# Optimization experiments

Hardware: AMD Instinct MI355X
Metric: run time of the kernel (lower is better)

The kernel has to match this reference:

```python
import jax, jax.numpy as jnp
import numpy as np
import math

INF = 1e10

def setup_inputs() -> dict:
    key = jax.random.key(0)
    ks = jax.random.split(key, 6)
    B, S, T, D = 8, 1024, 1024, 1024
    stdv = 1.0 / math.sqrt(D)
    return {
        "key": jax.random.normal(ks[0], (B, S, D), dtype=jnp.float32),
        "mask_src": jnp.ones((B, S), dtype=jnp.float32),
        "mask_trg": jnp.ones((B, T), dtype=jnp.float32),
        "Wq": jax.random.uniform(ks[1], (D, D), jnp.float32, -stdv, stdv),
        "bq": jnp.zeros((D,), jnp.float32),
        "Wk": jax.random.uniform(ks[2], (D, D), jnp.float32, -stdv, stdv),
        "bk": jnp.zeros((D,), jnp.float32),
        "wg": jax.random.uniform(ks[3], (D,), jnp.float32, -stdv, stdv),
        "bg": jnp.zeros((1,), jnp.float32),
    }


def reference(key, mask_src, mask_trg, Wq, bq, Wk, bk, wg, bg):
    B, S, D = key.shape
    T = mask_trg.shape[1]
    scale = jnp.asarray(math.sqrt(D), key.dtype)

    # --- linear (position-based Gaussian) attention ---
    src_lens = mask_src.sum(-1)                      # [B]
    trg_lens = mask_trg.sum(-1)                      # [B]
    steps = src_lens / trg_lens                      # [B]
    idx_t = steps[:, None] * jnp.arange(T, dtype=key.dtype)[None, :]   # [B,T]
    idx_s = jnp.arange(S, dtype=key.dtype)                              # [S]
    dist2 = (idx_s[None, None, :] - idx_t[:, :, None]) ** 2            # [B,T,S]
    l_logits = -dist2 / 0.3 - INF * (1.0 - mask_src[:, None, :])
    l_att = jax.nn.softmax(l_logits, axis=-1)                           # [B,T,S]

    # query from position attention
    query = jnp.einsum('bts,bsd->btd', l_att, key)                      # [B,T,D]

    # learned gate, broadcast [B,T,1] -> [B,T,S]
    gates = jax.nn.sigmoid(query @ wg + bg)[:, :, None]                 # [B,T,1]

    # QK dot-product attention
    q = query @ Wq.T + bq                                               # [B,T,D]
    k = key @ Wk.T + bk                                                 # [B,S,D]
    dots = jnp.einsum('btd,bsd->bts', q, k)
    dots = dots - (1.0 - mask_src[:, None, :]) * INF
    probs = jax.nn.softmax(dots / scale, axis=-1)                       # [B,T,S]

    # gated mixture of QK attention and position attention
    return (1.0 - gates) * probs + gates * l_att
```

## Files before the change

kernel.cpp:

```cpp
#include <hip/hip_runtime.h>
#include <hip/hip_bf16.h>
#include <stdint.h>

typedef unsigned short ushort_t;

#define BB 8
#define SS 1024
#define TT 1024
#define DD 1024
#define INF_ 1e10f

__device__ __forceinline__ float b2f(ushort_t u){
  union { unsigned u32; float f; } x; x.u32 = ((unsigned)u) << 16; return x.f;
}
__device__ __forceinline__ ushort_t f2b(float f){
  union { float f; unsigned u; } x; x.f = f;
  unsigned r = x.u + 0x7FFFu + ((x.u >> 16) & 1u);
  return (ushort_t)(r >> 16);
}

__global__ __launch_bounds__(256) void pre_kernel(
    const float* __restrict__ Wq, const float* __restrict__ Wk,
    ushort_t* __restrict__ WqT, ushort_t* __restrict__ WkT,
    const float* __restrict__ msrc, const float* __restrict__ mtrg,
    float* __restrict__ steps, float* __restrict__ v2)
{
  __shared__ float tile[32][33];
  __shared__ float sh[8];
  int blk = blockIdx.x, tid = threadIdx.x;
  if (blk < 2048){
    const float* src = (blk >= 1024) ? Wk : Wq;
    ushort_t* dst = (blk >= 1024) ? WkT : WqT;
    int q = blk & 1023;
    int tx = q & 31, ty = q >> 5;
    int c = tid & 31, r0 = tid >> 5;
    #pragma unroll
    for (int k = 0; k < 4; k++){
      int r = r0 + k*8;
      tile[r][c] = src[(size_t)(ty*32 + r)*DD + tx*32 + c];
    }
    __syncthreads();
    #pragma unroll
    for (int k = 0; k < 4; k++){
      int r = r0 + k*8;
      dst[(size_t)(tx*32 + r)*DD + ty*32 + c] = f2b(tile[c][r]);
    }
  } else {
    int b = blk - 2048;
    if (b < 4) v2[b*256 + tid] = 0.f;
    float a = 0.f, c = 0.f;
    for (int i = tid; i < SS; i += 256) a += msrc[b*SS + i];
    for (int i = tid; i < TT; i += 256) c += mtrg[b*TT + i];
    #pragma unroll
    for (int o = 32; o; o >>= 1){ a += __shfl_xor(a, o); c += __shfl_xor(c, o); }
    int wv = tid >> 6, ln = tid & 63;
    if (!ln){ sh[wv] = a; sh[4+wv] = c; }
    __syncthreads();
    if (!tid){
      float sa = sh[0]+sh[1]+sh[2]+sh[3];
      float sc = sh[4]+sh[5]+sh[6]+sh[7];
      steps[b] = sa / sc;
    }
  }
}

__global__ __launch_bounds__(256) void v2_kernel(
    const float* __restrict__ Wk, const float* __restrict__ bq,
    float* __restrict__ v2)
{
  int tid = threadIdx.x;
  int f = tid * 4;
  int r0 = blockIdx.x * 32;
  float a0=0.f, a1=0.f, a2=0.f, a3=0.f;
  for (int r = 0; r < 32; r++){
    float s = bq[r0 + r];
    float4 w = *(const float4*)(Wk + (size_t)(r0 + r)*DD + f);
    a0 += s*w.x; a1 += s*w.y; a2 += s*w.z; a3 += s*w.w;
  }
  atomicAdd(&v2[f+0], a0); atomicAdd(&v2[f+1], a1);
  atomicAdd(&v2[f+2], a2); atomicAdd(&v2[f+3], a3);
}

__global__ __launch_bounds__(256) void key_convert_kernel(
    const float* __restrict__ key, const float* __restrict__ wg,
    const float* __restrict__ v2f, ushort_t* __restrict__ keyb,
    float* __restrict__ kw, float* __restrict__ cv)
{
  __shared__ float sh[8];
  int row = blockIdx.x;
  int tid = threadIdx.x, d0 = tid*4;
  float4 v = *(const float4*)(key + (size_t)row*DD + d0);
  ushort4 o; o.x=f2b(v.x); o.y=f2b(v.y); o.z=f2b(v.z); o.w=f2b(v.w);
  *(ushort4*)(keyb + (size_t)row*DD + d0) = o;
  float4 w4 = *(const float4*)(wg + d0);
  float4 u4 = *(const float4*)(v2f + d0);
  float pk = v.x*w4.x + v.y*w4.y + v.z*w4.z + v.w*w4.w;
  float pc = v.x*u4.x + v.y*u4.y + v.z*u4.z + v.w*u4.w;
  #pragma unroll
  for (int off = 32; off; off >>= 1){ pk += __shfl_xor(pk, off); pc += __shfl_xor(pc, off); }
  int wvv = tid >> 6;
  if ((tid & 63) == 0){ sh[wvv] = pk; sh[4+wvv] = pc; }
  __syncthreads();
  if (!tid){
    kw[row] = sh[0]+sh[1]+sh[2]+sh[3];
    cv[row] = sh[4]+sh[5]+sh[6]+sh[7];
  }
}

typedef __bf16 bf16x8 __attribute__((ext_vector_type(8)));
typedef float f32x4 __attribute__((ext_vector_type(4)));

#define CP16(g, l) __builtin_amdgcn_global_load_lds( \
    (const __attribute__((address_space(1))) void*)(g), \
    (__attribute__((address_space(3))) void*)(l), 16, 0, 0)

__global__ __launch_bounds__(256, 2) void gemm_bt_kernel(
    const ushort_t* __restrict__ A, const ushort_t* __restrict__ Bm,
    const float* __restrict__ bias, void* __restrict__ Cv,
    int M, int N, int K, int lda, int ldb,
    long long sA, long long sB, long long sC, int hasBias, int outBF16,
    int gx, int gxy)
{
  __shared__ ushort_t lA[128*32];
  __shared__ ushort_t lB[128*32];

  const int bpx = gridDim.x >> 3;
  const int lin = blockIdx.x;
  const int glob = (lin & 7) * bpx + (lin >> 3);
  const int bz = glob / gxy;
  const int rem = glob - bz * gxy;
  const int by = rem / gx;
  const int bx = rem - by * gx;

  A  += (size_t)bz * sA;
  Bm += (size_t)bz * sB;

  const int tid = threadIdx.x;
  const int wv = tid >> 6, ln = tid & 63;
  const int r4 = ln >> 2, c8 = (ln & 3) * 8;

  const ushort_t* gA0 = A  + (size_t)(by*128 + wv*32 + r4) * lda + c8;
  const ushort_t* gA1 = gA0 + (size_t)16 * lda;
  const ushort_t* gB0 = Bm + (size_t)(bx*128 + wv*32 + r4) * ldb + c8;
  const ushort_t* gB1 = gB0 + (size_t)16 * ldb;
  ushort_t* lA0 = &lA[(wv*32     ) * 32];
  ushort_t* lA1 = &lA[(wv*32 + 16) * 32];
  ushort_t* lB0 = &lB[(wv*32     ) * 32];
  ushort_t* lB1 = &lB[(wv*32 + 16) * 32];

  const int lm = ln & 15, qd = ln >> 4;
  const int wm = (wv >> 1) * 64, wn = (wv & 1) * 64;

  f32x4 acc[4][4];
  #pragma unroll
  for (int i = 0; i < 4; i++)
    #pragma unroll
    for (int j = 0; j < 4; j++) acc[i][j] = (f32x4){0.f, 0.f, 0.f, 0.f};

  for (int k0 = 0; k0 < K; k0 += 32){
    CP16(gA0, lA0); CP16(gA1, lA1); CP16(gB0, lB0); CP16(gB1, lB1);
    gA0 += 32; gA1 += 32; gB0 += 32; gB1 += 32;
    __syncthreads();
    bf16x8 af[4], bf[4];
    #pragma unroll
    for (int i = 0; i < 4; i++) af[i] = *(const bf16x8*)&lA[(wm + i*16 + lm)*32 + qd*8];
    #pragma unroll
    for (int j = 0; j < 4; j++) bf[j] = *(const bf16x8*)&lB[(wn + j*16 + lm)*32 + qd*8];
    #pragma unroll
    for (int i = 0; i < 4; i++)
      #pragma unroll
      for (int j = 0; j < 4; j++)
        acc[i][j] = __builtin_amdgcn_mfma_f32_16x16x32_bf16(af[i], bf[j], acc[i][j], 0, 0, 0);
    __syncthreads();
  }

  const int row0 = by*128 + wm + qd*4;
  const int col0 = bx*128 + wn + lm;
  ushort_t* Cb = (ushort_t*)Cv + (size_t)bz * sC;
  float*    Cf = (float*)Cv    + (size_t)bz * sC;
  #pragma unroll
  for (int j = 0; j < 4; j++){
    int col = col0 + j*16;
    float bv = hasBias ? bias[col] : 0.f;
    #pragma unroll
    for (int i = 0; i < 4; i++)
      #pragma unroll
      for (int r = 0; r < 4; r++){
        size_t idx = (size_t)(row0 + i*16 + r) * N + col;
        float v = acc[i][j][r] + bv;
        if (outBF16) Cb[idx] = f2b(v); else Cf[idx] = v;
      }
  }
}

__global__ __launch_bounds__(256) void wmt_reduce_kernel(
    const float* __restrict__ part, ushort_t* __restrict__ dst)
{
  int i4 = blockIdx.x * 256 + threadIdx.x;
  const float4* p = (const float4*)part;
  float4 a = p[i4];
  float4 b = p[i4 + 262144];
  float4 c = p[i4 + 524288];
  float4 d = p[i4 + 786432];
  ushort4 o;
  o.x = f2b(a.x + b.x + c.x + d.x);
  o.y = f2b(a.y + b.y + c.y + d.y);
  o.z = f2b(a.z + b.z + c.z + d.z);
  o.w = f2b(a.w + b.w + c.w + d.w);
  ((ushort4*)dst)[i4] = o;
}

__global__ __launch_bounds__(256) void band_kernel(
    const ushort_t* __restrict__ kmb, const float* __restrict__ mask_src,
    const float* __restrict__ steps, const float* __restrict__ kw,
    const float* __restrict__ bg, ushort_t* __restrict__ qm2b,
    float* __restrict__ gates)
{
  __shared__ float shw[8][17];
  __shared__ int shslo[8];
  int bx = blockIdx.x;
  int b = bx >> 7, t0 = (bx & 127) * 8;
  int tid = threadIdx.x;

  if (tid < 8){
    int t = t0 + tid;
    float c = steps[b] * (float)t;
    int slo = (int)ceilf(c - 8.0f);
    float w[17], m = -3e38f;
    #pragma unroll
    for (int i = 0; i < 17; i++){
      int s = slo + i;
      float l = -3e38f;
      if (s >= 0 && s < SS){
        float dd = (float)s - c;
        l = -dd*dd*(1.0f/0.3f) - INF_*(1.0f - mask_src[b*SS + s]);
      }
      w[i] = l; m = fmaxf(m, l);
    }
    float norm = 0.f, ga = 0.f;
    #pragma unroll
    for (int i = 0; i < 17; i++){
      float e = __expf(w[i] - m);
      int s = slo + i;
      if (s >= 0 && s < SS) ga += e * kw[b*SS + s]; else e = 0.f;
      w[i] = e; norm += e;
    }
    float inv = 1.0f / norm;
    #pragma unroll
    for (int i = 0; i < 17; i++) shw[tid][i] = w[i] * inv;
    shslo[tid] = slo;
    gates[b*TT + t] = 1.0f / (1.0f + __expf(-(ga*inv + bg[0])));
  }
  __syncthreads();

  int smin = shslo[0], smax = shslo[7] + 16;
  if (smin < 0) smin = 0;
  if (smax > SS-1) smax = SS-1;
  int d0 = tid * 4;
  float acc[8][4];
  #pragma unroll
  for (int t = 0; t < 8; t++){ acc[t][0]=0.f; acc[t][1]=0.f; acc[t][2]=0.f; acc[t][3]=0.f; }

  const ushort_t* kbase = kmb + ((size_t)b*SS)*DD + d0;
  for (int s = smin; s <= smax; s++){
    ushort4 kv = *(const ushort4*)(kbase + (size_t)s*DD);
    float k0 = b2f(kv.x), k1 = b2f(kv.y), k2 = b2f(kv.z), k3 = b2f(kv.w);
    #pragma unroll
    for (int t = 0; t < 8; t++){
      unsigned u = (unsigned)(s - shslo[t]);
      if (u < 17u){
        float wgt = shw[t][u];
        acc[t][0] += wgt*k0; acc[t][1] += wgt*k1; acc[t][2] += wgt*k2; acc[t][3] += wgt*k3;
      }
    }
  }
  #pragma unroll
  for (int t = 0; t < 8; t++){
    ushort4 o; o.x=f2b(acc[t][0]); o.y=f2b(acc[t][1]); o.z=f2b(acc[t][2]); o.w=f2b(acc[t][3]);
    *(ushort4*)(qm2b + ((size_t)(b*TT + t0 + t))*DD + d0) = o;
  }
}

__device__ __forceinline__ float blkmax(float v, float* sh){
  #pragma unroll
  for (int o = 32; o; o >>= 1) v = fmaxf(v, __shfl_xor(v, o));
  __syncthreads();
  if ((threadIdx.x & 63) == 0) sh[threadIdx.x >> 6] = v;
  __syncthreads();
  return fmaxf(fmaxf(sh[0], sh[1]), fmaxf(sh[2], sh[3]));
}
__device__ __forceinline__ float blksum(float v, float* sh){
  #pragma unroll
  for (int o = 32; o; o >>= 1) v += __shfl_xor(v, o);
  __syncthreads();
  if ((threadIdx.x & 63) == 0) sh[threadIdx.x >> 6] = v;
  __syncthreads();
  return sh[0] + sh[1] + sh[2] + sh[3];
}

__global__ __launch_bounds__(256) void softmax_mix_kernel(
    const ushort_t* __restrict__ dotsb, float* __restrict__ out,
    const float* __restrict__ mask_src, const float* __restrict__ steps,
    const float* __restrict__ gates, const float* __restrict__ cv)
{
  __shared__ float sh[4];
  int blk = blockIdx.x;
  int b = blk >> 10, t = blk & 1023;
  int tid = threadIdx.x;
  int s0 = tid * 4;
  float c = steps[b] * (float)t;

  ushort4 dv = *(const ushort4*)(dotsb + (size_t)blk*SS + s0);
  float4 mv = *(const float4*)(mask_src + (size_t)b*SS + s0);
  float4 cva = *(const float4*)(cv + (size_t)b*SS + s0);
  float dvf[4] = {b2f(dv.x) + cva.x, b2f(dv.y) + cva.y, b2f(dv.z) + cva.z, b2f(dv.w) + cva.w};
  float msk[4] = {mv.x, mv.y, mv.z, mv.w};
  float dl[4], ll[4];
  float dmax = -3e38f, lmax = -3e38f;
  #pragma unroll
  for (int r = 0; r < 4; r++){
    float im = INF_ * (1.0f - msk[r]);
    dl[r] = (dvf[r] - im) * (1.0f/32.0f);
    float dd = (float)(s0 + r) - c;
    ll[r] = -dd*dd*(1.0f/0.3f) - im;
    dmax = fmaxf(dmax, dl[r]);
    lmax = fmaxf(lmax, ll[r]);
  }
  float dm = blkmax(dmax, sh);
  float ps[4], lp[4];
  float psum = 0.f, lsum = 0.f;
  #pragma unroll
  for (int r = 0; r < 4; r++){ ps[r] = __expf(dl[r] - dm); psum += ps[r]; }
  psum = blksum(psum, sh);
  float lm2 = blkmax(lmax, sh);
  #pragma unroll
  for (int r = 0; r < 4; r++){ lp[r] = __expf(ll[r] - lm2); lsum += lp[r]; }
  lsum = blksum(lsum, sh);

  float g = gates[blk];
  float ip = (1.0f - g) / psum, il = g / lsum;
  float4 ov;
  ov.x = ps[0]*ip + lp[0]*il;
  ov.y = ps[1]*ip + lp[1]*il;
  ov.z = ps[2]*ip + lp[2]*il;
  ov.w = ps[3]*ip + lp[3]*il;
  *(float4*)(out + (size_t)blk*SS + s0) = ov;
}

extern "C" void kernel_launch(void* const* d_in, const int* in_sizes, int n_in,
                              void* d_out, int out_size, void* d_ws, size_t ws_size,
                              hipStream_t stream)
{
  const float* key      = (const float*)d_in[0];
  const float* mask_src = (const float*)d_in[1];
  const float* mask_trg = (const float*)d_in[2];
  const float* Wq       = (const float*)d_in[3];
  const float* bq       = (const float*)d_in[4];
  const float* Wk       = (const float*)d_in[5];
  const float* bk       = (const float*)d_in[6];
  const float* wg       = (const float*)d_in[7];
  const float* bg       = (const float*)d_in[8];
  float* out = (float*)d_out;
  (void)bk;

  char* ws = (char*)d_ws;
  float* steps     = (float*)ws;
  float* gates     = (float*)(ws + 4096);
  float* cv        = (float*)(ws + 4096 + 32768);
  float* kw        = (float*)(ws + 4096 + 65536);
  float* v2        = (float*)(ws + 4096 + 98304);
  ushort_t* WqTb   = (ushort_t*)(ws + 131072);
  ushort_t* WkTb   = WqTb + (size_t)DD*DD;
  ushort_t* WmTb   = WkTb + (size_t)DD*DD;
  ushort_t* keyb   = WmTb + (size_t)DD*DD;
  ushort_t* kmb    = keyb + (size_t)BB*SS*DD;
  char* shared16   = (char*)(kmb + (size_t)BB*SS*DD);
  float* wmPart    = (float*)shared16;
  ushort_t* qm2b   = (ushort_t*)shared16;
  ushort_t* dotsb  = kmb;

  pre_kernel<<<2056, 256, 0, stream>>>(Wq, Wk, WqTb, WkTb, mask_src, mask_trg, steps, v2);
  v2_kernel<<<32, 256, 0, stream>>>(Wk, bq, v2);
  key_convert_kernel<<<BB*SS, 256, 0, stream>>>(key, wg, v2, keyb, kw, cv);
  gemm_bt_kernel<<<256, 256, 0, stream>>>(
      WkTb, WqTb, nullptr, (void*)wmPart, DD, DD, DD/4, DD, DD,
      DD/4, DD/4, (long long)DD*DD, 0, 0, 8, 64);
  wmt_reduce_kernel<<<DD*DD/4/256, 256, 0, stream>>>(wmPart, WmTb);
  gemm_bt_kernel<<<512, 256, 0, stream>>>(
      keyb, WmTb, nullptr, (void*)kmb, BB*SS, DD, DD, DD, DD, 0, 0, 0, 0, 1, 8, 512);
  band_kernel<<<BB*TT/8, 256, 0, stream>>>(kmb, mask_src, steps, kw, bg, qm2b, gates);
  gemm_bt_kernel<<<512, 256, 0, stream>>>(
      qm2b, keyb, nullptr, (void*)dotsb, TT, SS, DD, DD, DD,
      (long long)TT*DD, (long long)SS*DD, (long long)TT*SS, 0, 1, 8, 64);
  softmax_mix_kernel<<<BB*TT, 256, 0, stream>>>(dotsb, out, mask_src, steps, gates, cv);
}
```

Before: 216.7 us.

## Add 256x128-tile GEMM kernel with 3-stage A pipeline for large GEMMs

Adds a new bf16 MFMA GEMM kernel that uses 512 threads, 256x128 output tiles, triple-buffered A and double-buffered B LDS staging with XOR swizzle, and an XCD-aware block remap. It replaces the two large GEMMs (key x Wm and q x key dots) that previously used the 128x128 gemm_bt_kernel. The larger tile raises arithmetic intensity and cuts global traffic per flop. In exchange the grid drops to 256 blocks with higher register and LDS use per block, which lowers occupancy.

```diff
diff --git a/kernel.cpp b/kernel.cpp
--- a/kernel.cpp
+++ b/kernel.cpp
@@ -191,6 +191,105 @@
         if (outBF16) Cb[idx] = f2b(v); else Cf[idx] = v;
       }
   }
+}
+
+#define G2_STAGE_A(sel, k0) do{ \
+    ushort_t* _d = &lA3[(sel)*(256*64) + (w*8)*64]; \
+    CP16(gA0 + (k0), _d); \
+    CP16(gA1 + (k0), _d + 64*64); \
+    CP16(gA2 + (k0), _d + 128*64); \
+    CP16(gA3 + (k0), _d + 192*64); }while(0)
+#define G2_STAGE_B(sel, k0) do{ \
+    ushort_t* _d = &lB2[(sel)*(128*64) + (w*8)*64]; \
+    CP16(gB0 + (k0), _d); \
+    CP16(gB1 + (k0), _d + 64*64); }while(0)
+
+__global__ __launch_bounds__(512, 2) void gemm256_kernel(
+    const ushort_t* __restrict__ A, const ushort_t* __restrict__ Bm,
+    ushort_t* __restrict__ C,
+    int M, int N, int K, int lda, int ldb,
+    long long sA, long long sB, long long sC, int gx, int gxy)
+{
+  __shared__ ushort_t lA3[3 * 256 * 64];
+  __shared__ ushort_t lB2[2 * 128 * 64];
+  (void)M;
+
+  const int bpx = gridDim.x >> 3;
+  const int lin = blockIdx.x;
+  const int glob = (lin & 7) * bpx + (lin >> 3);
+  const int bz = glob / gxy;
+  const int rem = glob - bz * gxy;
+  const int by = rem / gx;
+  const int bx = rem - by * gx;
+
+  A  += (size_t)bz * sA;
+  Bm += (size_t)bz * sB;
+
+  const int tid = threadIdx.x;
+  const int w = tid >> 6, l = tid & 63;
+  const int lm = l & 15, qd = l >> 4;
+  const int wm = w >> 2, wn = w & 3;
+
+  const int srow = l >> 3;
+  const int sch  = (l & 7) ^ srow;
+
+  const ushort_t* gA0 = A + (size_t)(by*256 +       w*8 + srow) * lda + sch*8;
+  const ushort_t* gA1 = gA0 + (size_t)64  * lda;
+  const ushort_t* gA2 = gA0 + (size_t)128 * lda;
+  const ushort_t* gA3 = gA0 + (size_t)192 * lda;
+  const ushort_t* gB0 = Bm + (size_t)(bx*128 +      w*8 + srow) * ldb + sch*8;
+  const ushort_t* gB1 = gB0 + (size_t)64  * ldb;
+
+  f32x4 acc[8][2];
+  #pragma unroll
+  for (int i = 0; i < 8; i++){ acc[i][0] = (f32x4){0.f,0.f,0.f,0.f}; acc[i][1] = (f32x4){0.f,0.f,0.f,0.f}; }
+
+  G2_STAGE_A(0, 0);
+  G2_STAGE_B(0, 0);
+  G2_STAGE_A(1, 64);
+
+  const int NT = K >> 6;
+  int rdA = 0, stA = 2, rdB = 0;
+  for (int t = 0; t < NT; ++t){
+    if (t < NT - 1) asm volatile("s_waitcnt vmcnt(4)" ::: "memory");
+    else            asm volatile("s_waitcnt vmcnt(0)" ::: "memory");
+    __builtin_amdgcn_s_barrier();
+    if (t + 1 < NT) G2_STAGE_B(rdB ^ 1, (t+1)*64);
+    if (t + 2 < NT) G2_STAGE_A(stA,     (t+2)*64);
+
+    const ushort_t* sa = &lA3[rdA*(256*64) + (wm*128)*64];
+    const ushort_t* sb = &lB2[rdB*(128*64) + (wn*32)*64];
+    #pragma unroll
+    for (int ks = 0; ks < 2; ++ks){
+      const int ch = ((ks << 2) | qd) ^ (lm & 7);
+      bf16x8 af[8], bfr[2];
+      #pragma unroll
+      for (int i = 0; i < 8; i++) af[i]  = *(const bf16x8*)&sa[(i*16 + lm)*64 + ch*8];
+      #pragma unroll
+      for (int j = 0; j < 2; j++) bfr[j] = *(const bf16x8*)&sb[(j*16 + lm)*64 + ch*8];
+      __builtin_amdgcn_s_setprio(1);
+      #pragma unroll
+      for (int i = 0; i < 8; i++)
+        #pragma unroll
+        for (int j = 0; j < 2; j++)
+          acc[i][j] = __builtin_amdgcn_mfma_f32_16x16x32_bf16(af[i], bfr[j], acc[i][j], 0, 0, 0);
+      __builtin_amdgcn_s_setprio(0);
+    }
+    rdA = (rdA == 2) ? 0 : rdA + 1;
+    stA = (stA == 2) ? 0 : stA + 1;
+    rdB ^= 1;
+  }
+
+  const int row0 = by*256 + wm*128 + qd*4;
+  const int col0 = bx*128 + wn*32 + lm;
+  ushort_t* Cp = C + (size_t)bz * sC;
+  #pragma unroll
+  for (int j = 0; j < 2; j++)
+    #pragma unroll
+    for (int i = 0; i < 8; i++)
+      #pragma unroll
+      for (int r = 0; r < 4; r++)
+        Cp[(size_t)(row0 + i*16 + r) * N + col0 + j*16] = f2b(acc[i][j][r]);
 }
 
 __global__ __launch_bounds__(256) void wmt_reduce_kernel(
@@ -386,11 +485,11 @@
       WkTb, WqTb, nullptr, (void*)wmPart, DD, DD, DD/4, DD, DD,
       DD/4, DD/4, (long long)DD*DD, 0, 0, 8, 64);
   wmt_reduce_kernel<<<DD*DD/4/256, 256, 0, stream>>>(wmPart, WmTb);
-  gemm_bt_kernel<<<512, 256, 0, stream>>>(
-      keyb, WmTb, nullptr, (void*)kmb, BB*SS, DD, DD, DD, DD, 0, 0, 0, 0, 1, 8, 512);
+  gemm256_kernel<<<256, 512, 0, stream>>>(
+      keyb, WmTb, kmb, BB*SS, DD, DD, DD, DD, 0, 0, 0, 8, 256);
   band_kernel<<<BB*TT/8, 256, 0, stream>>>(kmb, mask_src, steps, kw, bg, qm2b, gates);
-  gemm_bt_kernel<<<512, 256, 0, stream>>>(
-      qm2b, keyb, nullptr, (void*)dotsb, TT, SS, DD, DD, DD,
-      (long long)TT*DD, (long long)SS*DD, (long long)TT*SS, 0, 1, 8, 64);
+  gemm256_kernel<<<256, 512, 0, stream>>>(
+      qm2b, keyb, dotsb, TT, SS, DD, DD, DD,
+      (long long)TT*DD, (long long)SS*DD, (long long)TT*SS, 8, 32);
   softmax_mix_kernel<<<BB*TT, 256, 0, stream>>>(dotsb, out, mask_src, steps, gates, cv);
 }
```

Measured after the change: 221.8 us. +2.3%, slower.
